# Performance work log

Hardware: AMD Instinct MI355X
Metric: run time of the kernel (lower is better)

## Reference

```python
import jax, jax.numpy as jnp
import numpy as np

N_NODES = 1024
NUM_MOL = 32
ATOMS = 32          # atoms per molecule
SDIM = 256
VDIM = 64
EDIM = 128
NUM_BOND_TYPES = 5


def _fully_connected_edges():
    # all ordered pairs (j, i), j != i, within each molecule block
    idx = np.arange(ATOMS)
    jj, ii = np.meshgrid(idx, idx, indexing='ij')
    mask = jj != ii
    jj, ii = jj[mask], ii[mask]                      # [ATOMS*(ATOMS-1)]
    offs = (np.arange(NUM_MOL) * ATOMS)[:, None]
    j_all = (jj[None, :] + offs).reshape(-1)
    i_all = (ii[None, :] + offs).reshape(-1)
    return np.stack([j_all, i_all]).astype(np.int32)  # [2, E]


def setup_inputs() -> dict:
    key = jax.random.key(0)
    ks = jax.random.split(key, 12)
    edge_index = jnp.asarray(_fully_connected_edges())  # [2, 31744]
    E = edge_index.shape[1]
    inp = {
        's': jax.random.normal(ks[0], (N_NODES, SDIM), jnp.float32),
        'v': jax.random.normal(ks[1], (N_NODES, 3, VDIM), jnp.float32),
        'p': jax.random.normal(ks[2], (N_NODES, 3), jnp.float32),
        'e': jax.random.normal(ks[3], (E, EDIM), jnp.float32),
        'batch': jnp.repeat(jnp.arange(NUM_MOL, dtype=jnp.int32), ATOMS),
        'edge_index': edge_index,
        # learned parameters
        'W_shared': jax.random.normal(ks[4], (SDIM, SDIM), jnp.float32) * 0.02,
        'b_shared': jnp.zeros((SDIM,), jnp.float32),
        'W_coords': jax.random.normal(ks[5], (VDIM, 1), jnp.float32) * 0.02,
        'W_bond': jax.random.normal(ks[6], (EDIM, SDIM), jnp.float32) * 0.02,
        'b_bond': jnp.zeros((SDIM,), jnp.float32),
        'W_b0': jax.random.normal(ks[7], (SDIM + 1, SDIM), jnp.float32) * 0.02,
        'b_b0': jnp.zeros((SDIM,), jnp.float32),
        'W_b1': jax.random.normal(ks[8], (SDIM, NUM_BOND_TYPES), jnp.float32) * 0.02,
        'b_b1': jnp.zeros((NUM_BOND_TYPES,), jnp.float32),
    }
    return inp


def reference(s, v, p, e, batch, edge_index,
              W_shared, b_shared, W_coords, W_bond, b_bond,
              W_b0, b_b0, W_b1, b_b1):
    n = s.shape[0]
    # shared_mapping: DenseLayer with SiLU
    s = jax.nn.silu(s @ W_shared + b_shared)
    # coords_lin: [n,3,vdim] @ [vdim,1] -> [n,3]
    coords = p + jnp.einsum('ncv,vo->nc', v, W_coords)
    # scatter_mean centering per molecule
    seg_sum = jax.ops.segment_sum(coords, batch, num_segments=NUM_MOL)
    counts = jax.ops.segment_sum(jnp.ones((n, 1), coords.dtype), batch,
                                 num_segments=NUM_MOL)
    mean = seg_sum / jnp.maximum(counts, 1.0)
    coords = coords - mean[batch]
    # dense symmetrization of edge features
    j, i = edge_index[0], edge_index[1]
    e_dense = jnp.zeros((n, n, e.shape[-1]), e.dtype).at[j, i].set(e)
    e_dense = 0.5 * (e_dense + jnp.swapaxes(e_dense, 0, 1))
    e_sym = e_dense[j, i]                                  # [E, EDIM]
    # squared distance per edge
    d = jnp.sum((coords[i] - coords[j]) ** 2, axis=-1, keepdims=True)  # [E,1]
    # edge MLP
    f = s[i] + s[j] + (e_sym @ W_bond + b_bond)            # [E, SDIM]
    edge = jnp.concatenate([f, d], axis=-1)                # [E, SDIM+1]
    h = jax.nn.silu(edge @ W_b0 + b_b0)
    bonds_pred = h @ W_b1 + b_b1                           # [E, 5]
    return bonds_pred
```

## Files before the change

kernel.cpp:

```cpp
#include <hip/hip_runtime.h>
#include <hip/hip_bf16.h>

#define N_NODES 1024
#define NUM_MOL 32
#define ATOMS 32
#define SDIM 256
#define VDIM 64
#define EDIM 128
#define NBT 5
#define EDGES_PER_MOL (ATOMS * (ATOMS - 1))
#define PAIRS_PER_MOL (ATOMS * (ATOMS - 1) / 2)
#define N_PAIRS (NUM_MOL * PAIRS_PER_MOL)

typedef __attribute__((ext_vector_type(8))) short bf16x8;
typedef __attribute__((ext_vector_type(4))) float f32x4;

__device__ __forceinline__ unsigned short f2bf(float x) {
    union { float f; unsigned int u; } v; v.f = x;
    unsigned int r = v.u + 0x7fffu + ((v.u >> 16) & 1u);
    return (unsigned short)(r >> 16);
}

__device__ __forceinline__ bf16x8 pack8(const float4& x0, const float4& x1) {
    bf16x8 r;
    r[0] = (short)f2bf(x0.x); r[1] = (short)f2bf(x0.y);
    r[2] = (short)f2bf(x0.z); r[3] = (short)f2bf(x0.w);
    r[4] = (short)f2bf(x1.x); r[5] = (short)f2bf(x1.y);
    r[6] = (short)f2bf(x1.z); r[7] = (short)f2bf(x1.w);
    return r;
}

__global__ __launch_bounds__(256) void misc_kernel(
    const float* __restrict__ s, const float* __restrict__ Ws,
    const float* __restrict__ bs, const float* __restrict__ Wb0,
    const float* __restrict__ v, const float* __restrict__ p,
    const float* __restrict__ Wc,
    const float* __restrict__ Wbond, const float* __restrict__ bbond,
    const float* __restrict__ bb0,
    float* __restrict__ sp2, float* __restrict__ coords,
    unsigned short* __restrict__ Wf, float* __restrict__ bcomb)
{
    __shared__ __align__(16) float smem[4096];
    const int t   = threadIdx.x;
    const int bid = blockIdx.x;

    if (bid < 64) {
        unsigned short* s2u = (unsigned short*)smem;
        const int w  = t >> 6, l = t & 63;
        const int kg = l >> 4, lr = l & 15;
        const int r0 = bid * 16;

        bf16x8 a[8];
        const float* srow = s + (size_t)(r0 + lr) * SDIM + kg * 8;
#pragma unroll
        for (int kt = 0; kt < 8; ++kt) {
            const float4 x0 = *(const float4*)(srow + kt * 32);
            const float4 x1 = *(const float4*)(srow + kt * 32 + 4);
            a[kt] = pack8(x0, x1);
        }

        f32x4 acc[4];
#pragma unroll
        for (int q = 0; q < 4; ++q) {
            acc[q][0] = 0.f; acc[q][1] = 0.f; acc[q][2] = 0.f; acc[q][3] = 0.f;
            const int n = (w * 4 + q) * 16 + lr;
            const float* wcol = Ws + n;
#pragma unroll
            for (int kt = 0; kt < 8; ++kt) {
                const int kbase = kt * 32 + kg * 8;
                bf16x8 bf;
#pragma unroll
                for (int e2 = 0; e2 < 8; ++e2)
                    bf[e2] = (short)f2bf(wcol[(size_t)(kbase + e2) * SDIM]);
                acc[q] = __builtin_amdgcn_mfma_f32_16x16x32_bf16(a[kt], bf, acc[q], 0, 0, 0);
            }
        }

#pragma unroll
        for (int q = 0; q < 4; ++q) {
            const int n = (w * 4 + q) * 16 + lr;
            const float bsv = bs[n];
#pragma unroll
            for (int j = 0; j < 4; ++j) {
                const int row = kg * 4 + j;
                const float x = acc[q][j] + bsv;
                const float sl = x / (1.f + __expf(-x));
                s2u[(row * 256 + n) ^ ((row & 7) << 3)] = f2bf(sl);
            }
        }
        __syncthreads();

#pragma unroll
        for (int kt = 0; kt < 8; ++kt) {
            const int idx = (lr * 256 + kt * 32 + kg * 8) ^ ((lr & 7) << 3);
            a[kt] = *(const bf16x8*)&s2u[idx];
        }

#pragma unroll
        for (int q = 0; q < 4; ++q) {
            acc[q][0] = 0.f; acc[q][1] = 0.f; acc[q][2] = 0.f; acc[q][3] = 0.f;
            const int n = (w * 4 + q) * 16 + lr;
            const float* wcol = Wb0 + n;
#pragma unroll
            for (int kt = 0; kt < 8; ++kt) {
                const int kbase = kt * 32 + kg * 8;
                bf16x8 bf;
#pragma unroll
                for (int e2 = 0; e2 < 8; ++e2)
                    bf[e2] = (short)f2bf(wcol[(size_t)(kbase + e2) * SDIM]);
                acc[q] = __builtin_amdgcn_mfma_f32_16x16x32_bf16(a[kt], bf, acc[q], 0, 0, 0);
            }
        }
#pragma unroll
        for (int q = 0; q < 4; ++q) {
            const int n = (w * 4 + q) * 16 + lr;
#pragma unroll
            for (int j = 0; j < 4; ++j) {
                const int row = kg * 4 + j;
                sp2[(size_t)(r0 + row) * SDIM + n] = acc[q][j];
            }
        }

    } else if (bid < 96) {
        const int mol = bid - 64;
        float* cl   = smem;
        float* mean = smem + 100;
        if (t < ATOMS * 3) {
            const int a = t / 3, dim = t % 3;
            const int node = mol * ATOMS + a;
            const float* vv = v + (size_t)node * 3 * VDIM + dim * VDIM;
            float acc = 0.f;
#pragma unroll 8
            for (int k = 0; k < VDIM; ++k) acc += vv[k] * Wc[k];
            cl[a * 3 + dim] = p[node * 3 + dim] + acc;
        }
        __syncthreads();
        if (t < 3) {
            float sum = 0.f;
            for (int a = 0; a < ATOMS; ++a) sum += cl[a * 3 + t];
            mean[t] = sum * (1.f / ATOMS);
        }
        __syncthreads();
        if (t < ATOMS * 3) {
            const int a = t / 3, dim = t % 3;
            coords[(mol * ATOMS + a) * 3 + dim] = cl[a * 3 + dim] - mean[dim];
        }

    } else if (bid < 128) {
        float (*wb)[SDIM] = (float (*)[SDIM])smem;
        const int r0 = (bid - 96) * 4;
        for (int r = 0; r < 4; ++r) wb[r][t] = Wbond[(r0 + r) * SDIM + t];
        __syncthreads();

        float acc[4];
#pragma unroll
        for (int r = 0; r < 4; ++r) acc[r] = 0.f;
        for (int c = 0; c < SDIM; c += 4) {
            const float w0 = Wb0[(c + 0) * SDIM + t];
            const float w1 = Wb0[(c + 1) * SDIM + t];
            const float w2 = Wb0[(c + 2) * SDIM + t];
            const float w3 = Wb0[(c + 3) * SDIM + t];
#pragma unroll
            for (int r = 0; r < 4; ++r) {
                const float4 wv = *(const float4*)&wb[r][c];
                acc[r] += wv.x * w0 + wv.y * w1 + wv.z * w2 + wv.w * w3;
            }
        }
        const int nt = t >> 4;
#pragma unroll
        for (int r = 0; r < 4; ++r) {
            const int k = r0 + r;
            const int kt = k >> 5, g = (k >> 3) & 3, eidx = k & 7;
            const int lane = (t & 15) + 16 * g;
            Wf[((size_t)((nt * 4 + kt) * 64 + lane)) * 8 + eidx] = f2bf(0.5f * acc[r]);
        }
    } else {
        float acc = bb0[t];
#pragma unroll 8
        for (int m = 0; m < SDIM; ++m) acc += bbond[m] * Wb0[m * SDIM + t];
        bcomb[t] = acc;
    }
}

#define PB 16
__global__ __launch_bounds__(256) void edge_mfma_kernel(
    const float* __restrict__ sp2, const float* __restrict__ coords,
    const float* __restrict__ e, const unsigned short* __restrict__ Wf,
    const float* __restrict__ bcomb, const float* __restrict__ Wb0,
    const float* __restrict__ Wb1, const float* __restrict__ bb1,
    float* __restrict__ out)
{
    __shared__ __align__(16) float spsum[PB][260];
    __shared__ __align__(16) unsigned short esym[PB * EDIM];
    __shared__ float wb1s[SDIM * NBT];
    __shared__ float bb1s[8];
    __shared__ int   ksh[PB], krevsh[PB], ish[PB], jsh[PB];
    __shared__ float dsh[PB];

    const int t  = threadIdx.x;
    const int P0 = blockIdx.x * PB;

    for (int idx = t; idx < SDIM * NBT; idx += 256) wb1s[idx] = Wb1[idx];
    if (t < NBT) bb1s[t] = bb1[t];
    if (t < PB) {
        const int P   = P0 + t;
        const int mol = P / PAIRS_PER_MOL;
        const int p   = P - mol * PAIRS_PER_MOL;
        int jj = (int)((63.0f - sqrtf((float)(3969 - 8 * p))) * 0.5f);
        if (jj < 0) jj = 0;
        if (jj > 30) jj = 30;
        while (jj > 0 && (63 * jj - jj * jj) / 2 > p) --jj;
        while (jj < 30 && (63 * (jj + 1) - (jj + 1) * (jj + 1)) / 2 <= p) ++jj;
        const int Ojj = (63 * jj - jj * jj) / 2;
        const int ii  = jj + 1 + (p - Ojj);
        const int q    = jj * 31 + (ii - 1);
        const int qrev = ii * 31 + jj;
        ksh[t]    = mol * EDGES_PER_MOL + q;
        krevsh[t] = mol * EDGES_PER_MOL + qrev;
        const int i = mol * ATOMS + ii, j = mol * ATOMS + jj;
        ish[t] = i; jsh[t] = j;
        const float dx = coords[i * 3 + 0] - coords[j * 3 + 0];
        const float dy = coords[i * 3 + 1] - coords[j * 3 + 1];
        const float dz = coords[i * 3 + 2] - coords[j * 3 + 2];
        dsh[t] = dx * dx + dy * dy + dz * dz;
    }
    __syncthreads();

    {
        const int r  = t >> 4;
        const int c8 = (t & 15) * 8;
        const float* ek  = e + (size_t)ksh[r] * EDIM + c8;
        const float* ekr = e + (size_t)krevsh[r] * EDIM + c8;
        const float4 x0 = *(const float4*)(ek);
        const float4 x1 = *(const float4*)(ek + 4);
        const float4 y0 = *(const float4*)(ekr);
        const float4 y1 = *(const float4*)(ekr + 4);

        const int c0 = (t & 15) * 4;
        const float* ai = sp2 + (size_t)ish[r] * SDIM;
        const float* aj = sp2 + (size_t)jsh[r] * SDIM;
        const float* w2 = Wb0 + (size_t)SDIM * SDIM;
        const float d = dsh[r];
#pragma unroll
        for (int i = 0; i < 4; ++i) {
            const int c = c0 + 64 * i;
            const float4 a4 = *(const float4*)(ai + c);
            const float4 b4 = *(const float4*)(aj + c);
            const float4 w4 = *(const float4*)(w2 + c);
            const float4 g4 = *(const float4*)(bcomb + c);
            float4 rv;
            rv.x = a4.x + b4.x + d * w4.x + g4.x;
            rv.y = a4.y + b4.y + d * w4.y + g4.y;
            rv.z = a4.z + b4.z + d * w4.z + g4.z;
            rv.w = a4.w + b4.w + d * w4.w + g4.w;
            *(float4*)&spsum[r][c] = rv;
        }

        float4 sx, sy;
        sx.x = x0.x + y0.x; sx.y = x0.y + y0.y; sx.z = x0.z + y0.z; sx.w = x0.w + y0.w;
        sy.x = x1.x + y1.x; sy.y = x1.y + y1.y; sy.z = x1.z + y1.z; sy.w = x1.w + y1.w;
        const int idx = (r * EDIM + c8) ^ ((r & 7) << 3);
        *(bf16x8*)&esym[idx] = pack8(sx, sy);
    }
    __syncthreads();

    const int w = t >> 6, l = t & 63;
    const int kg = l >> 4, lr = l & 15;

    bf16x8 afrag[4];
#pragma unroll
    for (int kt = 0; kt < 4; ++kt) {
        const int idx = (lr * EDIM + kt * 32 + kg * 8) ^ ((lr & 7) << 3);
        afrag[kt] = *(const bf16x8*)&esym[idx];
    }

    const bf16x8* wfp = (const bf16x8*)Wf;
    f32x4 acc[4];
#pragma unroll
    for (int q = 0; q < 4; ++q) {
        acc[q][0] = 0.f; acc[q][1] = 0.f; acc[q][2] = 0.f; acc[q][3] = 0.f;
        const int nt = w * 4 + q;
        const bf16x8 b0 = wfp[(nt * 4 + 0) * 64 + l];
        const bf16x8 b1 = wfp[(nt * 4 + 1) * 64 + l];
        const bf16x8 b2 = wfp[(nt * 4 + 2) * 64 + l];
        const bf16x8 b3 = wfp[(nt * 4 + 3) * 64 + l];
        acc[q] = __builtin_amdgcn_mfma_f32_16x16x32_bf16(afrag[0], b0, acc[q], 0, 0, 0);
        acc[q] = __builtin_amdgcn_mfma_f32_16x16x32_bf16(afrag[1], b1, acc[q], 0, 0, 0);
        acc[q] = __builtin_amdgcn_mfma_f32_16x16x32_bf16(afrag[2], b2, acc[q], 0, 0, 0);
        acc[q] = __builtin_amdgcn_mfma_f32_16x16x32_bf16(afrag[3], b3, acc[q], 0, 0, 0);
    }

#pragma unroll
    for (int q = 0; q < 4; ++q) {
        const int n = (w * 4 + q) * 16 + lr;
#pragma unroll
        for (int j = 0; j < 4; ++j) {
            const int r = kg * 4 + j;
            const float x = acc[q][j] + spsum[r][n];
            spsum[r][n] = x / (1.f + __expf(-x));
        }
    }
    __syncthreads();

    if (t < PB * NBT * 2) {
        const int task = t >> 1, half = t & 1;
        const int r  = task / NBT;
        const int tt = task - r * NBT;
        float a = half ? 0.f : bb1s[tt];
        const int base = half * 32;
#pragma unroll 4
        for (int cc = 0; cc < 32; ++cc) {
            const int c4 = base + ((cc + task) & 31);
            const int c  = c4 * 4;
            const float4 hv = *(const float4*)&spsum[r][c];
            a += hv.x * wb1s[(c + 0) * NBT + tt] + hv.y * wb1s[(c + 1) * NBT + tt] +
                 hv.z * wb1s[(c + 2) * NBT + tt] + hv.w * wb1s[(c + 3) * NBT + tt];
        }
        a += __shfl_xor(a, 1);
        if (!half) {
            out[(size_t)ksh[r] * NBT + tt]    = a;
            out[(size_t)krevsh[r] * NBT + tt] = a;
        }
    }
}

extern "C" void kernel_launch(void* const* d_in, const int* in_sizes, int n_in,
                              void* d_out, int out_size, void* d_ws, size_t ws_size,
                              hipStream_t stream)
{
    const float* s        = (const float*)d_in[0];
    const float* v        = (const float*)d_in[1];
    const float* p        = (const float*)d_in[2];
    const float* e        = (const float*)d_in[3];
    const float* W_shared = (const float*)d_in[6];
    const float* b_shared = (const float*)d_in[7];
    const float* W_coords = (const float*)d_in[8];
    const float* W_bond   = (const float*)d_in[9];
    const float* b_bond   = (const float*)d_in[10];
    const float* W_b0     = (const float*)d_in[11];
    const float* b_b0     = (const float*)d_in[12];
    const float* W_b1     = (const float*)d_in[13];
    const float* b_b1     = (const float*)d_in[14];
    float* out = (float*)d_out;

    float* sp2    = (float*)d_ws;
    float* coords = sp2 + (size_t)N_NODES * SDIM;
    unsigned short* Wf = (unsigned short*)(coords + 3072);
    float* bcomb  = (float*)((char*)Wf + 65536);

    misc_kernel<<<129, 256, 0, stream>>>(s, W_shared, b_shared, W_b0,
                                         v, p, W_coords,
                                         W_bond, b_bond, b_b0,
                                         sp2, coords, Wf, bcomb);
    edge_mfma_kernel<<<N_PAIRS / PB, 256, 0, stream>>>(sp2, coords, e, Wf, bcomb,
                                                       W_b0, W_b1, b_b1, out);
}
```

Before: 30.00 us.

## Split node GEMMs into prepack stage and MFMA-fragment node kernel; swizzle edge blocks

Splits the old misc kernel into a prep kernel that converts W_shared, W_b0 and s into bf16 in MFMA fragment order, and a separate node kernel that runs the two chained GEMMs from those prepacked, coalesced fragments. Previously each of the 64 node blocks gathered strided fp32 weight columns and converted them itself, so every block redundantly reloaded and converted the full weight matrices. The edge kernel also remaps its block index so that consecutive launched blocks are spread across pair ranges. The cost is one extra kernel launch and a serial dependency between prep and node stages.

```diff
diff --git a/kernel.cpp b/kernel.cpp
--- a/kernel.cpp
+++ b/kernel.cpp
@@ -30,99 +30,79 @@
     return r;
 }
 
-__global__ __launch_bounds__(256) void misc_kernel(
+__global__ __launch_bounds__(256) void prep_kernel(
     const float* __restrict__ s, const float* __restrict__ Ws,
-    const float* __restrict__ bs, const float* __restrict__ Wb0,
+    const float* __restrict__ Wb0,
+    const float* __restrict__ Wbond, const float* __restrict__ bbond,
+    const float* __restrict__ bb0,
     const float* __restrict__ v, const float* __restrict__ p,
     const float* __restrict__ Wc,
-    const float* __restrict__ Wbond, const float* __restrict__ bbond,
-    const float* __restrict__ bb0,
-    float* __restrict__ sp2, float* __restrict__ coords,
-    unsigned short* __restrict__ Wf, float* __restrict__ bcomb)
+    unsigned short* __restrict__ Wsf, unsigned short* __restrict__ Wb0f,
+    unsigned short* __restrict__ sbf, unsigned short* __restrict__ Wf,
+    float* __restrict__ bcomb, float* __restrict__ coords)
 {
-    __shared__ __align__(16) float smem[4096];
+    __shared__ __align__(16) float smem[1024 + 16];
     const int t   = threadIdx.x;
     const int bid = blockIdx.x;
 
     if (bid < 64) {
-        unsigned short* s2u = (unsigned short*)smem;
-        const int w  = t >> 6, l = t & 63;
-        const int kg = l >> 4, lr = l & 15;
-        const int r0 = bid * 16;
-
-        bf16x8 a[8];
-        const float* srow = s + (size_t)(r0 + lr) * SDIM + kg * 8;
-#pragma unroll
-        for (int kt = 0; kt < 8; ++kt) {
-            const float4 x0 = *(const float4*)(srow + kt * 32);
-            const float4 x1 = *(const float4*)(srow + kt * 32 + 4);
-            a[kt] = pack8(x0, x1);
-        }
-
-        f32x4 acc[4];
-#pragma unroll
-        for (int q = 0; q < 4; ++q) {
-            acc[q][0] = 0.f; acc[q][1] = 0.f; acc[q][2] = 0.f; acc[q][3] = 0.f;
-            const int n = (w * 4 + q) * 16 + lr;
-            const float* wcol = Ws + n;
-#pragma unroll
-            for (int kt = 0; kt < 8; ++kt) {
-                const int kbase = kt * 32 + kg * 8;
-                bf16x8 bf;
-#pragma unroll
-                for (int e2 = 0; e2 < 8; ++e2)
-                    bf[e2] = (short)f2bf(wcol[(size_t)(kbase + e2) * SDIM]);
-                acc[q] = __builtin_amdgcn_mfma_f32_16x16x32_bf16(a[kt], bf, acc[q], 0, 0, 0);
+        const float* W = (bid < 32) ? Ws : Wb0;
+        unsigned short* dst = (bid < 32) ? Wsf : Wb0f;
+        const int g    = ((bid & 31) << 8) + t;
+        const int lane = g & 63;
+        const int kt   = (g >> 6) & 7;
+        const int nt   = g >> 9;
+        const int n     = nt * 16 + (lane & 15);
+        const int kbase = kt * 32 + (lane >> 4) * 8;
+        const float* col = W + (size_t)kbase * SDIM + n;
+        bf16x8 r;
+#pragma unroll
+        for (int e2 = 0; e2 < 8; ++e2) r[e2] = (short)f2bf(col[(size_t)e2 * SDIM]);
+        *(bf16x8*)&dst[(size_t)g * 8] = r;
+
+    } else if (bid < 192) {
+        const int g    = ((bid - 64) << 8) + t;
+        const int lane = g & 63;
+        const int kt   = (g >> 6) & 7;
+        const int rb   = g >> 9;
+        const int row   = rb * 16 + (lane & 15);
+        const int kbase = kt * 32 + (lane >> 4) * 8;
+        const float* srow = s + (size_t)row * SDIM + kbase;
+        const float4 x0 = *(const float4*)(srow);
+        const float4 x1 = *(const float4*)(srow + 4);
+        *(bf16x8*)&sbf[(size_t)g * 8] = pack8(x0, x1);
+
+    } else if (bid < 224) {
+        float (*wb)[SDIM] = (float (*)[SDIM])smem;
+        const int r0 = (bid - 192) * 4;
+        for (int r = 0; r < 4; ++r) wb[r][t] = Wbond[(r0 + r) * SDIM + t];
+        __syncthreads();
+
+        float acc[4];
+#pragma unroll
+        for (int r = 0; r < 4; ++r) acc[r] = 0.f;
+        for (int c = 0; c < SDIM; c += 4) {
+            const float w0 = Wb0[(c + 0) * SDIM + t];
+            const float w1 = Wb0[(c + 1) * SDIM + t];
+            const float w2 = Wb0[(c + 2) * SDIM + t];
+            const float w3 = Wb0[(c + 3) * SDIM + t];
+#pragma unroll
+            for (int r = 0; r < 4; ++r) {
+                const float4 wv = *(const float4*)&wb[r][c];
+                acc[r] += wv.x * w0 + wv.y * w1 + wv.z * w2 + wv.w * w3;
             }
         }
-
-#pragma unroll
-        for (int q = 0; q < 4; ++q) {
-            const int n = (w * 4 + q) * 16 + lr;
-            const float bsv = bs[n];
-#pragma unroll
-            for (int j = 0; j < 4; ++j) {
-                const int row = kg * 4 + j;
-                const float x = acc[q][j] + bsv;
-                const float sl = x / (1.f + __expf(-x));
-                s2u[(row * 256 + n) ^ ((row & 7) << 3)] = f2bf(sl);
-            }
-        }
-        __syncthreads();
-
-#pragma unroll
-        for (int kt = 0; kt < 8; ++kt) {
-            const int idx = (lr * 256 + kt * 32 + kg * 8) ^ ((lr & 7) << 3);
-            a[kt] = *(const bf16x8*)&s2u[idx];
-        }
-
-#pragma unroll
-        for (int q = 0; q < 4; ++q) {
-            acc[q][0] = 0.f; acc[q][1] = 0.f; acc[q][2] = 0.f; acc[q][3] = 0.f;
-            const int n = (w * 4 + q) * 16 + lr;
-            const float* wcol = Wb0 + n;
-#pragma unroll
-            for (int kt = 0; kt < 8; ++kt) {
-                const int kbase = kt * 32 + kg * 8;
-                bf16x8 bf;
-#pragma unroll
-                for (int e2 = 0; e2 < 8; ++e2)
-                    bf[e2] = (short)f2bf(wcol[(size_t)(kbase + e2) * SDIM]);
-                acc[q] = __builtin_amdgcn_mfma_f32_16x16x32_bf16(a[kt], bf, acc[q], 0, 0, 0);
-            }
-        }
-#pragma unroll
-        for (int q = 0; q < 4; ++q) {
-            const int n = (w * 4 + q) * 16 + lr;
-#pragma unroll
-            for (int j = 0; j < 4; ++j) {
-                const int row = kg * 4 + j;
-                sp2[(size_t)(r0 + row) * SDIM + n] = acc[q][j];
-            }
-        }
-
-    } else if (bid < 96) {
-        const int mol = bid - 64;
+        const int nt = t >> 4;
+#pragma unroll
+        for (int r = 0; r < 4; ++r) {
+            const int k = r0 + r;
+            const int kt = k >> 5, g = (k >> 3) & 3, eidx = k & 7;
+            const int lane = (t & 15) + 16 * g;
+            Wf[((size_t)((nt * 4 + kt) * 64 + lane)) * 8 + eidx] = f2bf(0.5f * acc[r]);
+        }
+
+    } else if (bid < 256) {
+        const int mol = bid - 224;
         float* cl   = smem;
         float* mean = smem + 100;
         if (t < ATOMS * 3) {
@@ -145,40 +125,83 @@
             const int a = t / 3, dim = t % 3;
             coords[(mol * ATOMS + a) * 3 + dim] = cl[a * 3 + dim] - mean[dim];
         }
-
-    } else if (bid < 128) {
-        float (*wb)[SDIM] = (float (*)[SDIM])smem;
-        const int r0 = (bid - 96) * 4;
-        for (int r = 0; r < 4; ++r) wb[r][t] = Wbond[(r0 + r) * SDIM + t];
-        __syncthreads();
-
-        float acc[4];
-#pragma unroll
-        for (int r = 0; r < 4; ++r) acc[r] = 0.f;
-        for (int c = 0; c < SDIM; c += 4) {
-            const float w0 = Wb0[(c + 0) * SDIM + t];
-            const float w1 = Wb0[(c + 1) * SDIM + t];
-            const float w2 = Wb0[(c + 2) * SDIM + t];
-            const float w3 = Wb0[(c + 3) * SDIM + t];
-#pragma unroll
-            for (int r = 0; r < 4; ++r) {
-                const float4 wv = *(const float4*)&wb[r][c];
-                acc[r] += wv.x * w0 + wv.y * w1 + wv.z * w2 + wv.w * w3;
-            }
-        }
-        const int nt = t >> 4;
-#pragma unroll
-        for (int r = 0; r < 4; ++r) {
-            const int k = r0 + r;
-            const int kt = k >> 5, g = (k >> 3) & 3, eidx = k & 7;
-            const int lane = (t & 15) + 16 * g;
-            Wf[((size_t)((nt * 4 + kt) * 64 + lane)) * 8 + eidx] = f2bf(0.5f * acc[r]);
-        }
     } else {
         float acc = bb0[t];
 #pragma unroll 8
         for (int m = 0; m < SDIM; ++m) acc += bbond[m] * Wb0[m * SDIM + t];
         bcomb[t] = acc;
+    }
+}
+
+__global__ __launch_bounds__(256) void node_kernel(
+    const unsigned short* __restrict__ sbf,
+    const unsigned short* __restrict__ Wsf,
+    const unsigned short* __restrict__ Wb0f,
+    const float* __restrict__ bs,
+    float* __restrict__ sp2)
+{
+    __shared__ __align__(16) unsigned short s2u[16 * 256];
+    const int t = threadIdx.x;
+    const int w = t >> 6, l = t & 63;
+    const int kg = l >> 4, lr = l & 15;
+    const int bid = blockIdx.x;
+    const int r0 = bid * 16;
+
+    const bf16x8* sfp = (const bf16x8*)sbf;
+    bf16x8 a[8];
+#pragma unroll
+    for (int kt = 0; kt < 8; ++kt) a[kt] = sfp[(bid * 8 + kt) * 64 + l];
+
+    const bf16x8* wsp = (const bf16x8*)Wsf;
+    f32x4 acc[4];
+#pragma unroll
+    for (int q = 0; q < 4; ++q) {
+        acc[q][0] = 0.f; acc[q][1] = 0.f; acc[q][2] = 0.f; acc[q][3] = 0.f;
+        const int nt = w * 4 + q;
+#pragma unroll
+        for (int kt = 0; kt < 8; ++kt) {
+            const bf16x8 bf = wsp[(nt * 8 + kt) * 64 + l];
+            acc[q] = __builtin_amdgcn_mfma_f32_16x16x32_bf16(a[kt], bf, acc[q], 0, 0, 0);
+        }
+    }
+
+#pragma unroll
+    for (int q = 0; q < 4; ++q) {
+        const int n = (w * 4 + q) * 16 + lr;
+        const float bsv = bs[n];
+#pragma unroll
+        for (int j = 0; j < 4; ++j) {
+            const int row = kg * 4 + j;
+            const float x = acc[q][j] + bsv;
+            const float sl = x / (1.f + __expf(-x));
+            s2u[(row * 256 + n) ^ ((row & 7) << 3)] = f2bf(sl);
+        }
+    }
+    __syncthreads();
+
+#pragma unroll
+    for (int kt = 0; kt < 8; ++kt) {
+        const int idx = (lr * 256 + kt * 32 + kg * 8) ^ ((lr & 7) << 3);
+        a[kt] = *(const bf16x8*)&s2u[idx];
+    }
+
+    const bf16x8* wbp = (const bf16x8*)Wb0f;
+#pragma unroll
+    for (int q = 0; q < 4; ++q) {
+        acc[q][0] = 0.f; acc[q][1] = 0.f; acc[q][2] = 0.f; acc[q][3] = 0.f;
+        const int nt = w * 4 + q;
+#pragma unroll
+        for (int kt = 0; kt < 8; ++kt) {
+            const bf16x8 bf = wbp[(nt * 8 + kt) * 64 + l];
+            acc[q] = __builtin_amdgcn_mfma_f32_16x16x32_bf16(a[kt], bf, acc[q], 0, 0, 0);
+        }
+    }
+#pragma unroll
+    for (int q = 0; q < 4; ++q) {
+        const int n = (w * 4 + q) * 16 + lr;
+#pragma unroll
+        for (int j = 0; j < 4; ++j)
+            sp2[(size_t)(r0 + kg * 4 + j) * SDIM + n] = acc[q][j];
     }
 }
 
@@ -197,8 +220,9 @@
     __shared__ int   ksh[PB], krevsh[PB], ish[PB], jsh[PB];
     __shared__ float dsh[PB];
 
-    const int t  = threadIdx.x;
-    const int P0 = blockIdx.x * PB;
+    const int t = threadIdx.x;
+    const int bid = (blockIdx.x & 7) * 124 + (blockIdx.x >> 3);
+    const int P0  = bid * PB;
 
     for (int idx = t; idx < SDIM * NBT; idx += 256) wb1s[idx] = Wb1[idx];
     if (t < NBT) bb1s[t] = bb1[t];
@@ -343,15 +367,19 @@
     const float* b_b1     = (const float*)d_in[14];
     float* out = (float*)d_out;
 
-    float* sp2    = (float*)d_ws;
-    float* coords = sp2 + (size_t)N_NODES * SDIM;
-    unsigned short* Wf = (unsigned short*)(coords + 3072);
-    float* bcomb  = (float*)((char*)Wf + 65536);
-
-    misc_kernel<<<129, 256, 0, stream>>>(s, W_shared, b_shared, W_b0,
+    char* ws = (char*)d_ws;
+    float*          sp2    = (float*)(ws + 0);
+    unsigned short* Wsf    = (unsigned short*)(ws + 1048576);
+    unsigned short* Wb0f   = (unsigned short*)(ws + 1179648);
+    unsigned short* sbf    = (unsigned short*)(ws + 1310720);
+    unsigned short* Wf     = (unsigned short*)(ws + 1835008);
+    float*          bcomb  = (float*)(ws + 1900544);
+    float*          coords = (float*)(ws + 1901568);
+
+    prep_kernel<<<257, 256, 0, stream>>>(s, W_shared, W_b0, W_bond, b_bond, b_b0,
                                          v, p, W_coords,
-                                         W_bond, b_bond, b_b0,
-                                         sp2, coords, Wf, bcomb);
+                                         Wsf, Wb0f, sbf, Wf, bcomb, coords);
+    node_kernel<<<64, 256, 0, stream>>>(sbf, Wsf, Wb0f, b_shared, sp2);
     edge_mfma_kernel<<<N_PAIRS / PB, 256, 0, stream>>>(sp2, coords, e, Wf, bcomb,
                                                        W_b0, W_b1, b_b1, out);
 }
```

Result: slower. 34.02 us (+13.4%).
